# Kernel tuning notes

Hardware: AMD Instinct MI355X
Metric: run time of the kernel (lower is better)

The kernel has to match this reference:

```python
import jax, jax.numpy as jnp
import numpy as np

B, T, DSEQ = 4096, 128, 128
DMEAN, DPRIOR = 256, 256
H, DOUT = 256, 128
NEXP, SCALE = 4, 0.1
NUM_EDGES = max(1, int(B * B * 0.05))  # static top-k size


def setup_inputs() -> dict:
    key = jax.random.key(0)
    ks = jax.random.split(key, 20)
    def n(k, shape):
        return jax.random.normal(k, shape, dtype=jnp.float32) * 0.02
    z = lambda *s: jnp.zeros(s, jnp.float32)
    return {
        "input_seq": jax.random.normal(ks[0], (B, T, DSEQ), dtype=jnp.float32),
        "mean_embedding": jax.random.normal(ks[1], (B, DMEAN), dtype=jnp.float32),
        "prior_target": jax.random.normal(ks[2], (B, DPRIOR), dtype=jnp.float32),
        "gru_Wih0": n(ks[3], (3 * H, DSEQ)), "gru_Whh0": n(ks[4], (3 * H, H)),
        "gru_bih0": z(3 * H), "gru_bhh0": z(3 * H),
        "gru_Wih1": n(ks[5], (3 * H, H)), "gru_Whh1": n(ks[6], (3 * H, H)),
        "gru_bih1": z(3 * H), "gru_bhh1": z(3 * H),
        "fc_mean_W": n(ks[7], (H, DMEAN)), "fc_mean_b": z(H),
        "gru_fc_W": n(ks[8], (DOUT, 2 * H)), "gru_fc_b": z(DOUT),
        "gcn1_W": n(ks[9], (H, DPRIOR)), "gcn1_b": z(H),
        "gcn2_W": n(ks[10], (H, H)), "gcn2_b": z(H),
        "prior_fc_W": n(ks[11], (DOUT, H)), "prior_fc_b": z(DOUT),
        "expert_W": n(ks[12], (NEXP, DOUT, DOUT)),
        "attn1_W": n(ks[13], (DOUT, 2 * DOUT)), "attn1_b": z(DOUT),
        "attn2_W": n(ks[14], (NEXP, DOUT)), "attn2_b": z(NEXP),
    }


def _gru_layer(x, Wih, Whh, bih, bhh):
    # x: [B,T,D]; PyTorch GRU cell equations
    h_dim = Whh.shape[1]
    def step(h, xt):
        gi = xt @ Wih.T + bih            # [B,3H]
        gh = h @ Whh.T + bhh
        i_r, i_z, i_n = jnp.split(gi, 3, axis=-1)
        h_r, h_z, h_n = jnp.split(gh, 3, axis=-1)
        r = jax.nn.sigmoid(i_r + h_r)
        zg = jax.nn.sigmoid(i_z + h_z)
        ng = jnp.tanh(i_n + r * h_n)
        h_new = (1.0 - zg) * ng + zg * h
        return h_new, h_new
    h0 = jnp.zeros((x.shape[0], h_dim), x.dtype)
    _, ys = jax.lax.scan(step, h0, jnp.swapaxes(x, 0, 1))
    return jnp.swapaxes(ys, 0, 1)


def _gcn(x, W, b, src, dst, n_nodes):
    # PyG GCNConv: add self-loops, sym-normalized mean aggregation
    loop = jnp.arange(n_nodes)
    s = jnp.concatenate([src, loop])
    d = jnp.concatenate([dst, loop])
    deg = jax.ops.segment_sum(jnp.ones(s.shape, x.dtype), d, num_segments=n_nodes)
    dinv = jnp.where(deg > 0, jax.lax.rsqrt(deg), 0.0)
    norm = dinv[s] * dinv[d]                  # [E]
    xw = x @ W.T                              # [N,H]
    out = jax.ops.segment_sum(xw[s] * norm[:, None], d, num_segments=n_nodes)
    return out + b


def reference(input_seq, mean_embedding, prior_target,
              gru_Wih0, gru_Whh0, gru_bih0, gru_bhh0,
              gru_Wih1, gru_Whh1, gru_bih1, gru_bhh1,
              fc_mean_W, fc_mean_b, gru_fc_W, gru_fc_b,
              gcn1_W, gcn1_b, gcn2_W, gcn2_b,
              prior_fc_W, prior_fc_b, expert_W,
              attn1_W, attn1_b, attn2_W, attn2_b):
    # --- GRU branch ---
    h1 = _gru_layer(input_seq, gru_Wih0, gru_Whh0, gru_bih0, gru_bhh0)
    h2 = _gru_layer(h1, gru_Wih1, gru_Whh1, gru_bih1, gru_bhh1)
    last_hidden = h2[:, -1, :]
    mean_feat = jax.nn.relu(mean_embedding @ fc_mean_W.T + fc_mean_b)
    gru_feat = jnp.concatenate([last_hidden, mean_feat], axis=1)
    gru_out_proj = gru_feat @ gru_fc_W.T + gru_fc_b          # [B,DOUT]
    # --- dynamic graph build via similarity top-k ---
    sim = prior_target @ prior_target.T                      # [B,B]
    diag = jnp.arange(B)
    sim = sim.at[diag, diag].set(0.0)
    _, topk_idx = jax.lax.top_k(sim.reshape(-1), NUM_EDGES)
    row = topk_idx // B
    col = topk_idx % B
    src = jnp.concatenate([row, col])   # symmetrized edge list
    dst = jnp.concatenate([col, row])
    # --- GCN branch ---
    ph = jax.nn.relu(_gcn(prior_target, gcn1_W, gcn1_b, src, dst, B))
    ph = jax.nn.relu(_gcn(ph, gcn2_W, gcn2_b, src, dst, B))
    prior_out = ph @ prior_fc_W.T + prior_fc_b               # [B,DOUT]
    # --- attention expert gate fusion ---
    base = 0.5 * gru_out_proj + 0.5 * prior_out
    diff = gru_out_proj - prior_out
    expert_res = jnp.einsum('eod,bd->beo', expert_W, diff)   # [B,NEXP,DOUT]
    fused = jnp.concatenate([gru_out_proj, prior_out], axis=-1)
    hatt = jnp.tanh(fused @ attn1_W.T + attn1_b)
    w = jax.nn.softmax(hatt @ attn2_W.T + attn2_b, axis=-1)  # [B,NEXP]
    delta = jnp.einsum('be,beo->bo', w, expert_res)
    pred = base + SCALE * delta
    return pred, gru_out_proj, prior_out
```

## Files before the change

### kernel.cpp

```cpp
#include <hip/hip_runtime.h>
#include <hip/hip_bf16.h>

#define BB    4096
#define TT    128
#define DSEQ_ 128
#define HH    256
#define DOUT_ 128
#define NEXP_ 4
static const long NUM_EDGES_ = 838860;

typedef _Float16 f16;
typedef _Float16 f16x8 __attribute__((ext_vector_type(8)));
typedef float    f32x4 __attribute__((ext_vector_type(4)));

#define GLL(gp, lp) __builtin_amdgcn_global_load_lds( \
    (const __attribute__((address_space(1))) void*)(gp), \
    (__attribute__((address_space(3))) void*)(lp), 16, 0, 0)

__global__ void pack_weights_kernel(const float* __restrict__ Wih,
                                    const float* __restrict__ Whh,
                                    f16* __restrict__ Wp, int Din)
{
    const int K = Din + HH;
    const int total = 1024 * K;
    for (int idx = blockIdx.x * 256 + threadIdx.x; idx < total; idx += gridDim.x * 256) {
        int n = idx / K, k = idx % K;
        int u = n >> 2, g = n & 3;
        float v = 0.f;
        if (k < Din) {
            if (g == 0)      v = Wih[(long)u * Din + k];
            else if (g == 1) v = Wih[(long)(256 + u) * Din + k];
            else if (g == 2) v = Wih[(long)(512 + u) * Din + k];
        } else {
            int kh = k - Din;
            if (g == 0)      v = Whh[(long)u * HH + kh];
            else if (g == 1) v = Whh[(long)(256 + u) * HH + kh];
            else if (g == 3) v = Whh[(long)(512 + u) * HH + kh];
        }
        Wp[idx] = (f16)v;
    }
}

__global__ void pack_bias_kernel(const float* __restrict__ bih,
                                 const float* __restrict__ bhh,
                                 float* __restrict__ bias)
{
    int n = blockIdx.x * 256 + threadIdx.x;
    if (n >= 1024) return;
    int u = n >> 2, g = n & 3;
    float v;
    if (g == 0)      v = bih[u] + bhh[u];
    else if (g == 1) v = bih[256 + u] + bhh[256 + u];
    else if (g == 2) v = bih[512 + u];
    else             v = bhh[512 + u];
    bias[n] = v;
}

__device__ __forceinline__ void mm_async(
    f32x4 (&acc)[4][4], f16* __restrict__ As, f16* __restrict__ Bs,
    const f16* __restrict__ Ag, long lda, const f16* __restrict__ Bg, long ldb,
    int kChunks, int wave, int lane)
{
    const int r0 = wave * 32 + (lane >> 2);
    const int ce = (lane & 3) * 8;
    const int wm = wave >> 1, wn = wave & 1;
    const int quad = lane >> 4, l15 = lane & 15;
    const f16* ag0 = Ag + (long)r0 * lda + ce;
    const f16* ag1 = ag0 + 16 * lda;
    const f16* bg0 = Bg + (long)r0 * ldb + ce;
    const f16* bg1 = bg0 + 16 * ldb;
    f16* asw = As + wave * 1024;
    f16* bsw = Bs + wave * 1024;
    for (int kc = 0; kc < kChunks; kc++) {
        __syncthreads();
        GLL(ag0, asw); GLL(ag1, asw + 512);
        GLL(bg0, bsw); GLL(bg1, bsw + 512);
        ag0 += 32; ag1 += 32; bg0 += 32; bg1 += 32;
        __syncthreads();
        f16x8 af[4], bf[4];
#pragma unroll
        for (int i = 0; i < 4; i++) {
            af[i] = *(const f16x8*)&As[(wm * 64 + i * 16 + l15) * 32 + quad * 8];
            bf[i] = *(const f16x8*)&Bs[(wn * 64 + i * 16 + l15) * 32 + quad * 8];
        }
#pragma unroll
        for (int mi = 0; mi < 4; mi++)
#pragma unroll
            for (int ni = 0; ni < 4; ni++)
                acc[mi][ni] = __builtin_amdgcn_mfma_f32_16x16x32_f16(af[mi], bf[ni], acc[mi][ni], 0, 0, 0);
    }
}

__global__ __launch_bounds__(256) void gru_superstep(
    const f16* __restrict__ Wp0, const float* __restrict__ bias0,
    const float* __restrict__ xseq,
    const f16* __restrict__ h1_in, f16* __restrict__ h1_out, int t0,
    const f16* __restrict__ Wp1, const float* __restrict__ bias1,
    const f16* __restrict__ h1_x,
    const f16* __restrict__ h2_in, f16* __restrict__ h2_out, int t1)
{
    const int layer = blockIdx.z;
    if (layer == 0 && t0 >= TT) return;
    if (layer == 1 && t1 < 0) return;

    __shared__ f16 As[4096];
    __shared__ f16 Bs[4096];
    const int tid = threadIdx.x;
    const int wave = tid >> 6, lane = tid & 63;
    const int wm = wave >> 1, wn = wave & 1;
    const int quad = lane >> 4, l15 = lane & 15;
    const long m0 = (long)blockIdx.x * 128;
    const int  n0 = blockIdx.y * 128;

    f32x4 acc[4][4];
#pragma unroll
    for (int i = 0; i < 4; i++)
#pragma unroll
        for (int j = 0; j < 4; j++) acc[i][j] = (f32x4){0.f, 0.f, 0.f, 0.f};

    const f16* hprev; f16* hout; const float* bias;
    if (layer == 0) {
        hprev = h1_in; hout = h1_out; bias = bias0;
        const int arow = tid >> 1, ac0 = (tid & 1) * 16;
        const float* ap = xseq + (m0 + arow) * ((long)TT * DSEQ_) + (long)t0 * DSEQ_ + ac0;
        const int r0 = wave * 32 + (lane >> 2);
        const int ce = (lane & 3) * 8;
        const f16* bg0 = Wp0 + (long)(n0 + r0) * 384 + ce;
        const f16* bg1 = bg0 + 16 * 384;
        f16* bsw = Bs + wave * 1024;
        for (int kc = 0; kc < 4; kc++) {
            float4 v0 = *(const float4*)(ap + 0);
            float4 v1 = *(const float4*)(ap + 4);
            float4 v2 = *(const float4*)(ap + 8);
            float4 v3 = *(const float4*)(ap + 12);
            ap += 32;
            __syncthreads();
            f16x8 w0, w1;
            w0[0] = (f16)v0.x; w0[1] = (f16)v0.y; w0[2] = (f16)v0.z; w0[3] = (f16)v0.w;
            w0[4] = (f16)v1.x; w0[5] = (f16)v1.y; w0[6] = (f16)v1.z; w0[7] = (f16)v1.w;
            w1[0] = (f16)v2.x; w1[1] = (f16)v2.y; w1[2] = (f16)v2.z; w1[3] = (f16)v2.w;
            w1[4] = (f16)v3.x; w1[5] = (f16)v3.y; w1[6] = (f16)v3.z; w1[7] = (f16)v3.w;
            *(f16x8*)&As[arow * 32 + ac0]     = w0;
            *(f16x8*)&As[arow * 32 + ac0 + 8] = w1;
            GLL(bg0, bsw); GLL(bg1, bsw + 512);
            bg0 += 32; bg1 += 32;
            __syncthreads();
            f16x8 af[4], bf[4];
#pragma unroll
            for (int i = 0; i < 4; i++) {
                af[i] = *(const f16x8*)&As[(wm * 64 + i * 16 + l15) * 32 + quad * 8];
                bf[i] = *(const f16x8*)&Bs[(wn * 64 + i * 16 + l15) * 32 + quad * 8];
            }
#pragma unroll
            for (int mi = 0; mi < 4; mi++)
#pragma unroll
                for (int ni = 0; ni < 4; ni++)
                    acc[mi][ni] = __builtin_amdgcn_mfma_f32_16x16x32_f16(af[mi], bf[ni], acc[mi][ni], 0, 0, 0);
        }
        mm_async(acc, As, Bs, h1_in + m0 * HH, HH, Wp0 + (long)n0 * 384 + 128, 384, 8, wave, lane);
    } else {
        hprev = h2_in; hout = h2_out; bias = bias1;
        mm_async(acc, As, Bs, h1_x + m0 * HH, HH, Wp1 + (long)n0 * 512, 512, 8, wave, lane);
        mm_async(acc, As, Bs, h2_in + m0 * HH, HH, Wp1 + (long)n0 * 512 + 256, 512, 8, wave, lane);
    }

    const long mbase = m0 + wm * 64;
    const int  nbase = n0 + wn * 64;
#pragma unroll
    for (int mi = 0; mi < 4; mi++) {
#pragma unroll
        for (int ni = 0; ni < 4; ni++) {
            const int ncol = nbase + ni * 16 + l15;
            const float bn = bias[ncol];
#pragma unroll
            for (int reg = 0; reg < 4; reg++) {
                float v = acc[mi][ni][reg] + bn;
                const int gb = lane & ~3;
                float g0 = __shfl(v, gb + 0, 64);
                float g1 = __shfl(v, gb + 1, 64);
                float g2 = __shfl(v, gb + 2, 64);
                float g3 = __shfl(v, gb + 3, 64);
                if ((lane & 3) == 0) {
                    const long mrow = mbase + mi * 16 + quad * 4 + reg;
                    const int u = ncol >> 2;
                    float hp = (float)hprev[mrow * HH + u];
                    float r = 1.f / (1.f + __expf(-g0));
                    float z = 1.f / (1.f + __expf(-g1));
                    float ng = 1.f - 2.f / (__expf(2.f * (g2 + r * g3)) + 1.f);
                    float hn = (1.f - z) * ng + z * hp;
                    hout[mrow * HH + u] = (f16)hn;
                }
            }
        }
    }
}

__global__ void sim_pack_kernel(const float* __restrict__ prior,
                                f16* __restrict__ pA, f16* __restrict__ pB)
{
    int i = blockIdx.x * 256 + threadIdx.x;
    if (i >= BB * 256) return;
    int b = i >> 8, k = i & 255;
    float v = prior[i];
    f16 hi = (f16)v;
    f16 lo = (f16)(v - (float)hi);
    long r = (long)b * 768;
    pA[r + k] = hi; pA[r + 256 + k] = hi; pA[r + 512 + k] = lo;
    pB[r + k] = hi; pB[r + 256 + k] = lo; pB[r + 512 + k] = hi;
}

__global__ __launch_bounds__(256) void sim_mm_kernel(
    const f16* __restrict__ pA, const f16* __restrict__ pB, float* __restrict__ sim)
{
    __shared__ f16 As[4096];
    __shared__ f16 Bs[4096];
    const int tid = threadIdx.x;
    const int wave = tid >> 6, lane = tid & 63;
    const int wm = wave >> 1, wn = wave & 1;
    const int quad = lane >> 4, l15 = lane & 15;
    const long m0 = (long)blockIdx.x * 128;
    const int  n0 = blockIdx.y * 128;
    f32x4 acc[4][4];
#pragma unroll
    for (int i = 0; i < 4; i++)
#pragma unroll
        for (int j = 0; j < 4; j++) acc[i][j] = (f32x4){0.f, 0.f, 0.f, 0.f};
    mm_async(acc, As, Bs, pA + m0 * 768, 768, pB + (long)n0 * 768, 768, 24, wave, lane);
    const long mbase = m0 + wm * 64;
    const int  nbase = n0 + wn * 64;
#pragma unroll
    for (int mi = 0; mi < 4; mi++)
#pragma unroll
        for (int ni = 0; ni < 4; ni++)
#pragma unroll
            for (int reg = 0; reg < 4; reg++) {
                long row = mbase + mi * 16 + quad * 4 + reg;
                int col = nbase + ni * 16 + l15;
                float v = acc[mi][ni][reg];
                if (row == (long)col) v = 0.f;
                sim[row * BB + col] = v;
            }
}

__device__ inline unsigned keyOf(float f)
{
    unsigned u = __float_as_uint(f);
    return (u & 0x80000000u) ? ~u : (u | 0x80000000u);
}

__global__ void hist_kernel(const float* __restrict__ sim, unsigned* __restrict__ hist,
                            const unsigned* __restrict__ state, int pass)
{
    __shared__ unsigned h[4096];
    for (int i = threadIdx.x; i < 4096; i += 256) h[i] = 0;
    __syncthreads();
    unsigned pfx1 = 0, pfx2 = 0;
    if (pass == 1) pfx1 = state[0];
    if (pass == 2) pfx2 = state[2];
    const long ntot = (long)BB * BB;
    for (long i = (long)blockIdx.x * 256 + threadIdx.x; i < ntot; i += (long)gridDim.x * 256) {
        unsigned key = keyOf(sim[i]);
        if (pass == 0) atomicAdd(&h[key >> 20], 1u);
        else if (pass == 1) { if ((key >> 20) == pfx1) atomicAdd(&h[(key >> 8) & 0xFFFu], 1u); }
        else               { if ((key >> 8) == pfx2)  atomicAdd(&h[key & 0xFFu], 1u); }
    }
    __syncthreads();
    const int nb = (pass == 2) ? 256 : 4096;
    for (int i = threadIdx.x; i < nb; i += 256)
        if (h[i]) atomicAdd(&hist[i], h[i]);
}

__global__ void scan_hist_kernel(const unsigned* __restrict__ hist,
                                 unsigned* __restrict__ state, int pass)
{
    __shared__ unsigned hl[4096];
    const int nb = (pass == 2) ? 256 : 4096;
    for (int i = threadIdx.x; i < nb; i += 256) hl[i] = hist[i];
    __syncthreads();
    if (threadIdx.x != 0 || blockIdx.x != 0) return;
    long k = (pass == 0) ? NUM_EDGES_ : (long)state[2 * pass - 1];
    long cum = 0; int b = nb - 1;
    for (; b >= 0; b--) { cum += hl[b]; if (cum >= k) break; }
    long kk = k - (cum - hl[b]);
    if (pass == 0) { state[0] = (unsigned)b; state[1] = (unsigned)kk; }
    else if (pass == 1) { state[2] = (state[0] << 12) | (unsigned)b; state[3] = (unsigned)kk; }
    else {
        unsigned key = (state[2] << 8) | (unsigned)b;
        state[4] = key;
        unsigned u = (key & 0x80000000u) ? (key ^ 0x80000000u) : ~key;
        state[5] = u;
    }
}

__global__ void degree_kernel(const float* __restrict__ sim, const unsigned* __restrict__ state,
                              float* __restrict__ dinv)
{
    const float thr = __uint_as_float(state[5]);
    const int d = blockIdx.x;
    const float* row = sim + (long)d * BB;
    int cnt = 0;
    for (int s = threadIdx.x; s < BB; s += 256) cnt += (row[s] >= thr) ? 1 : 0;
    for (int o = 32; o; o >>= 1) cnt += __shfl_down(cnt, o, 64);
    __shared__ int sh[4];
    if ((threadIdx.x & 63) == 0) sh[threadIdx.x >> 6] = cnt;
    __syncthreads();
    if (threadIdx.x == 0) {
        int tot = sh[0] + sh[1] + sh[2] + sh[3];
        dinv[d] = rsqrtf((float)(2 * tot + 1));
    }
}

__global__ void txp_kernel(const float* __restrict__ xws, f16* __restrict__ bT)
{
    int i = blockIdx.x * 256 + threadIdx.x;
    if (i >= BB * 256) return;
    int n = i >> 12, m = i & 4095;
    bT[(long)n * BB + m] = (f16)xws[(long)m * 256 + n];
}

__global__ __launch_bounds__(256) void gcn_mm_kernel(
    const float* __restrict__ sim, const f16* __restrict__ bT,
    const unsigned* __restrict__ state, float* __restrict__ ps)
{
    const float thr = __uint_as_float(state[5]);
    __shared__ f16 As[4096];
    __shared__ f16 Bs[4096];
    const int tid = threadIdx.x;
    const int wave = tid >> 6, lane = tid & 63;
    const int wm = wave >> 1, wn = wave & 1;
    const int quad = lane >> 4, l15 = lane & 15;
    const long m0 = (long)blockIdx.x * 128;
    const int  n0 = blockIdx.y * 128;
    const long kbase = (long)blockIdx.z * 1024;
    f32x4 acc[4][4];
#pragma unroll
    for (int i = 0; i < 4; i++)
#pragma unroll
        for (int j = 0; j < 4; j++) acc[i][j] = (f32x4){0.f, 0.f, 0.f, 0.f};

    const int arow = tid >> 1, ac0 = (tid & 1) * 16;
    const float* ap = sim + (m0 + arow) * (long)BB + kbase + ac0;
    const int r0 = wave * 32 + (lane >> 2);
    const int ce = (lane & 3) * 8;
    const f16* bg0 = bT + (long)(n0 + r0) * BB + kbase + ce;
    const f16* bg1 = bg0 + 16 * BB;
    f16* bsw = Bs + wave * 1024;
    const f16 one = (f16)1.f, zero = (f16)0.f;
    for (int kc = 0; kc < 32; kc++) {
        float4 v0 = *(const float4*)(ap + 0);
        float4 v1 = *(const float4*)(ap + 4);
        float4 v2 = *(const float4*)(ap + 8);
        float4 v3 = *(const float4*)(ap + 12);
        ap += 32;
        __syncthreads();
        f16x8 w0, w1;
        w0[0] = v0.x >= thr ? one : zero; w0[1] = v0.y >= thr ? one : zero;
        w0[2] = v0.z >= thr ? one : zero; w0[3] = v0.w >= thr ? one : zero;
        w0[4] = v1.x >= thr ? one : zero; w0[5] = v1.y >= thr ? one : zero;
        w0[6] = v1.z >= thr ? one : zero; w0[7] = v1.w >= thr ? one : zero;
        w1[0] = v2.x >= thr ? one : zero; w1[1] = v2.y >= thr ? one : zero;
        w1[2] = v2.z >= thr ? one : zero; w1[3] = v2.w >= thr ? one : zero;
        w1[4] = v3.x >= thr ? one : zero; w1[5] = v3.y >= thr ? one : zero;
        w1[6] = v3.z >= thr ? one : zero; w1[7] = v3.w >= thr ? one : zero;
        *(f16x8*)&As[arow * 32 + ac0]     = w0;
        *(f16x8*)&As[arow * 32 + ac0 + 8] = w1;
        GLL(bg0, bsw); GLL(bg1, bsw + 512);
        bg0 += 32; bg1 += 32;
        __syncthreads();
        f16x8 af[4], bf[4];
#pragma unroll
        for (int i = 0; i < 4; i++) {
            af[i] = *(const f16x8*)&As[(wm * 64 + i * 16 + l15) * 32 + quad * 8];
            bf[i] = *(const f16x8*)&Bs[(wn * 64 + i * 16 + l15) * 32 + quad * 8];
        }
#pragma unroll
        for (int mi = 0; mi < 4; mi++)
#pragma unroll
            for (int ni = 0; ni < 4; ni++)
                acc[mi][ni] = __builtin_amdgcn_mfma_f32_16x16x32_f16(af[mi], bf[ni], acc[mi][ni], 0, 0, 0);
    }
    const long mbase = m0 + wm * 64;
    const int  nbase = n0 + wn * 64;
    float* pbase = ps + (long)blockIdx.z * BB * 256;
#pragma unroll
    for (int mi = 0; mi < 4; mi++)
#pragma unroll
        for (int ni = 0; ni < 4; ni++)
#pragma unroll
            for (int reg = 0; reg < 4; reg++) {
                long row = mbase + mi * 16 + quad * 4 + reg;
                int col = nbase + ni * 16 + l15;
                pbase[row * 256 + col] = acc[mi][ni][reg];
            }
}

__global__ void gcn_combine_kernel(const float* __restrict__ ps, const float* __restrict__ xws,
                                   const float* __restrict__ dinv, const float* __restrict__ b,
                                   float* __restrict__ out)
{
    const long S = (long)BB * 256;
    long i = (long)blockIdx.x * 256 + threadIdx.x;
    if (i >= S) return;
    float s = ps[i] + ps[i + S] + ps[i + 2 * S] + ps[i + 3 * S];
    long m = i >> 8; int n = (int)(i & 255);
    out[i] = fmaxf(dinv[m] * (2.f * s + xws[i]) + b[n], 0.f);
}

__global__ __launch_bounds__(256) void gemm_bt_kernel(
    const float* __restrict__ A, const float* __restrict__ Bm, float* __restrict__ C,
    int M, int N, int K, const float* __restrict__ bias,
    const float* __restrict__ rscale, int act)
{
    __shared__ float As[16][65];
    __shared__ float Bs[16][65];
    const int tid = threadIdx.x;
    const long m0 = (long)blockIdx.x * 64;
    const int  n0 = blockIdx.y * 64;
    const int ty = tid >> 4, tx = tid & 15;
    const int mA = tid >> 2, kq = (tid & 3) * 4;
    float c[4][4] = {};
    for (int k0 = 0; k0 < K; k0 += 16) {
        __syncthreads();
        float4 va = *(const float4*)&A[(m0 + mA) * K + k0 + kq];
        As[kq + 0][mA] = va.x; As[kq + 1][mA] = va.y; As[kq + 2][mA] = va.z; As[kq + 3][mA] = va.w;
        float4 vb = *(const float4*)&Bm[(long)(n0 + mA) * K + k0 + kq];
        Bs[kq + 0][mA] = vb.x; Bs[kq + 1][mA] = vb.y; Bs[kq + 2][mA] = vb.z; Bs[kq + 3][mA] = vb.w;
        __syncthreads();
#pragma unroll
        for (int k = 0; k < 16; k++) {
            float a4[4], b4[4];
#pragma unroll
            for (int j = 0; j < 4; j++) { a4[j] = As[k][ty * 4 + j]; b4[j] = Bs[k][tx * 4 + j]; }
#pragma unroll
            for (int i = 0; i < 4; i++)
#pragma unroll
                for (int j = 0; j < 4; j++) c[i][j] = fmaf(a4[i], b4[j], c[i][j]);
        }
    }
#pragma unroll
    for (int i = 0; i < 4; i++) {
        const long m = m0 + ty * 4 + i;
        const float rs = rscale ? rscale[m] : 1.f;
#pragma unroll
        for (int j = 0; j < 4; j++) {
            const int n = n0 + tx * 4 + j;
            float v = c[i][j] * rs;
            if (bias) v += bias[n];
            if (act == 1) v = fmaxf(v, 0.f);
            else if (act == 2) v = tanhf(v);
            C[m * N + n] = v;
        }
    }
}

__global__ void build_gru_feat_kernel(const f16* __restrict__ h2, const float* __restrict__ mf,
                                      float* __restrict__ gf)
{
    long i = (long)blockIdx.x * 256 + threadIdx.x;
    if (i >= (long)BB * 512) return;
    long b = i >> 9; int c = (int)(i & 511);
    gf[i] = (c < 256) ? (float)h2[b * HH + c] : mf[b * HH + (c - 256)];
}

__global__ void build_fused_diff_kernel(const float* __restrict__ g, const float* __restrict__ p,
                                        float* __restrict__ fused, float* __restrict__ diff)
{
    long i = (long)blockIdx.x * 256 + threadIdx.x;
    if (i >= (long)BB * 256) return;
    long b = i >> 8; int c = (int)(i & 255);
    if (c < 128) {
        float gv = g[b * 128 + c], pv = p[b * 128 + c];
        fused[i] = gv;
        diff[b * 128 + c] = gv - pv;
    } else {
        fused[i] = p[b * 128 + (c - 128)];
    }
}

__global__ __launch_bounds__(128) void final_kernel(
    const float* __restrict__ hatt, const float* __restrict__ attn2W, const float* __restrict__ attn2b,
    const float* __restrict__ er, const float* __restrict__ g, const float* __restrict__ p,
    float* __restrict__ pred)
{
    const int b = blockIdx.x;
    __shared__ float w4[4];
    __shared__ float hrow[128];
    const int tid = threadIdx.x;
    hrow[tid] = hatt[(long)b * 128 + tid];
    __syncthreads();
    if (tid < 4) {
        float s = attn2b[tid];
        for (int d = 0; d < 128; d++) s += hrow[d] * attn2W[tid * 128 + d];
        w4[tid] = s;
    }
    __syncthreads();
    if (tid == 0) {
        float mx = fmaxf(fmaxf(w4[0], w4[1]), fmaxf(w4[2], w4[3]));
        float e0 = __expf(w4[0] - mx), e1 = __expf(w4[1] - mx);
        float e2 = __expf(w4[2] - mx), e3 = __expf(w4[3] - mx);
        float inv = 1.f / (e0 + e1 + e2 + e3);
        w4[0] = e0 * inv; w4[1] = e1 * inv; w4[2] = e2 * inv; w4[3] = e3 * inv;
    }
    __syncthreads();
    const long off = (long)b * 128 + tid;
    const long E = (long)BB * DOUT_;
    float base = 0.5f * g[off] + 0.5f * p[off];
    float delta = w4[0] * er[off] + w4[1] * er[off + E] + w4[2] * er[off + 2 * E] + w4[3] * er[off + 3 * E];
    pred[off] = base + 0.1f * delta;
}

extern "C" void kernel_launch(void* const* d_in, const int* in_sizes, int n_in,
                              void* d_out, int out_size, void* d_ws, size_t ws_size,
                              hipStream_t stream)
{
    const float* input_seq  = (const float*)d_in[0];
    const float* mean_emb   = (const float*)d_in[1];
    const float* prior      = (const float*)d_in[2];
    const float* Wih0       = (const float*)d_in[3];
    const float* Whh0       = (const float*)d_in[4];
    const float* bih0       = (const float*)d_in[5];
    const float* bhh0       = (const float*)d_in[6];
    const float* Wih1       = (const float*)d_in[7];
    const float* Whh1       = (const float*)d_in[8];
    const float* bih1       = (const float*)d_in[9];
    const float* bhh1       = (const float*)d_in[10];
    const float* fc_mean_W  = (const float*)d_in[11];
    const float* fc_mean_b  = (const float*)d_in[12];
    const float* gru_fc_W   = (const float*)d_in[13];
    const float* gru_fc_b   = (const float*)d_in[14];
    const float* gcn1_W     = (const float*)d_in[15];
    const float* gcn1_b     = (const float*)d_in[16];
    const float* gcn2_W     = (const float*)d_in[17];
    const float* gcn2_b     = (const float*)d_in[18];
    const float* prior_fc_W = (const float*)d_in[19];
    const float* prior_fc_b = (const float*)d_in[20];
    const float* expert_W   = (const float*)d_in[21];
    const float* attn1_W    = (const float*)d_in[22];
    const float* attn1_b    = (const float*)d_in[23];
    const float* attn2_W    = (const float*)d_in[24];
    const float* attn2_b    = (const float*)d_in[25];

    float* out_pred = (float*)d_out;
    float* out_g    = out_pred + (long)BB * DOUT_;
    float* out_p    = out_g + (long)BB * DOUT_;

    const size_t MB = 1u << 20;
    char* base = (char*)d_ws;
    size_t off = 0;
    auto alloc = [&](size_t bytes) -> char* {
        char* p = base + off;
        off = (off + bytes + 255) & ~(size_t)255;
        return p;
    };
    f16*   wp0    = (f16*)alloc((size_t)1024 * 384 * 2);
    f16*   wp1    = (f16*)alloc((size_t)1024 * 512 * 2);
    float* bias0  = (float*)alloc(1024 * 4);
    float* bias1  = (float*)alloc(1024 * 4);
    f16*   h1b[2]; h1b[0] = (f16*)alloc((size_t)BB * HH * 2); h1b[1] = (f16*)alloc((size_t)BB * HH * 2);
    f16*   h2b[2]; h2b[0] = (f16*)alloc((size_t)BB * HH * 2); h2b[1] = (f16*)alloc((size_t)BB * HH * 2);
    float* sim    = (float*)alloc((size_t)BB * BB * 4);
    unsigned* hist  = (unsigned*)alloc(4096 * 4);
    unsigned* state = (unsigned*)alloc(256);
    float* dinv   = (float*)alloc(BB * 4);
    float* xws1   = (float*)alloc((size_t)BB * HH * 4);
    float* ph1    = (float*)alloc((size_t)BB * HH * 4);
    float* xws2   = (float*)alloc((size_t)BB * HH * 4);
    float* ph2    = (float*)alloc((size_t)BB * HH * 4);
    f16*   xwsT16 = (f16*)alloc((size_t)256 * BB * 2);
    char*  region = alloc(20 * MB);
    if (off > ws_size) return;

    float* mf     = (float*)(region);
    float* gf     = (float*)(region + 5 * MB);
    f16*   packA  = (f16*)(region);
    f16*   packB  = (f16*)(region + 7 * MB);
    float* ps     = (float*)(region);
    float* diffb  = (float*)(region);
    float* fusedb = (float*)(region + 3 * MB);
    float* hatt   = (float*)(region + 8 * MB);
    float* er     = (float*)(region + 11 * MB);

    pack_weights_kernel<<<1536, 256, 0, stream>>>(Wih0, Whh0, wp0, DSEQ_);
    pack_weights_kernel<<<2048, 256, 0, stream>>>(Wih1, Whh1, wp1, HH);
    pack_bias_kernel<<<4, 256, 0, stream>>>(bih0, bhh0, bias0);
    pack_bias_kernel<<<4, 256, 0, stream>>>(bih1, bhh1, bias1);
    hipMemsetAsync(h1b[0], 0, (size_t)BB * HH * 2, stream);
    hipMemsetAsync(h1b[1], 0, (size_t)BB * HH * 2, stream);
    hipMemsetAsync(h2b[0], 0, (size_t)BB * HH * 2, stream);
    hipMemsetAsync(h2b[1], 0, (size_t)BB * HH * 2, stream);

    for (int tau = 0; tau <= TT; tau++) {
        gru_superstep<<<dim3(32, 8, 2), 256, 0, stream>>>(
            wp0, bias0, input_seq, h1b[tau & 1], h1b[(tau + 1) & 1], tau,
            wp1, bias1, h1b[tau & 1], h2b[tau & 1], h2b[(tau + 1) & 1], tau - 1);
    }
    const f16* h2fin = h2b[(TT + 1) & 1];

    gemm_bt_kernel<<<dim3(64, 4), 256, 0, stream>>>(mean_emb, fc_mean_W, mf, BB, HH, 256, fc_mean_b, nullptr, 1);
    build_gru_feat_kernel<<<(BB * 512) / 256, 256, 0, stream>>>(h2fin, mf, gf);
    gemm_bt_kernel<<<dim3(64, 2), 256, 0, stream>>>(gf, gru_fc_W, out_g, BB, DOUT_, 512, gru_fc_b, nullptr, 0);

    sim_pack_kernel<<<4096, 256, 0, stream>>>(prior, packA, packB);
    sim_mm_kernel<<<dim3(32, 32), 256, 0, stream>>>(packA, packB, sim);
    for (int pass = 0; pass < 3; pass++) {
        hipMemsetAsync(hist, 0, 4096 * 4, stream);
        hist_kernel<<<1024, 256, 0, stream>>>(sim, hist, state, pass);
        scan_hist_kernel<<<1, 256, 0, stream>>>(hist, state, pass);
    }
    degree_kernel<<<BB, 256, 0, stream>>>(sim, state, dinv);

    gemm_bt_kernel<<<dim3(64, 4), 256, 0, stream>>>(prior, gcn1_W, xws1, BB, HH, 256, nullptr, dinv, 0);
    txp_kernel<<<4096, 256, 0, stream>>>(xws1, xwsT16);
    gcn_mm_kernel<<<dim3(32, 2, 4), 256, 0, stream>>>(sim, xwsT16, state, ps);
    gcn_combine_kernel<<<4096, 256, 0, stream>>>(ps, xws1, dinv, gcn1_b, ph1);
    gemm_bt_kernel<<<dim3(64, 4), 256, 0, stream>>>(ph1, gcn2_W, xws2, BB, HH, 256, nullptr, dinv, 0);
    txp_kernel<<<4096, 256, 0, stream>>>(xws2, xwsT16);
    gcn_mm_kernel<<<dim3(32, 2, 4), 256, 0, stream>>>(sim, xwsT16, state, ps);
    gcn_combine_kernel<<<4096, 256, 0, stream>>>(ps, xws2, dinv, gcn2_b, ph2);
    gemm_bt_kernel<<<dim3(64, 2), 256, 0, stream>>>(ph2, prior_fc_W, out_p, BB, DOUT_, 256, prior_fc_b, nullptr, 0);

    build_fused_diff_kernel<<<(BB * 256) / 256, 256, 0, stream>>>(out_g, out_p, fusedb, diffb);
    for (int e = 0; e < NEXP_; e++)
        gemm_bt_kernel<<<dim3(64, 2), 256, 0, stream>>>(diffb, expert_W + (long)e * DOUT_ * DOUT_,
                                                        er + (long)e * BB * DOUT_, BB, DOUT_, DOUT_,
                                                        nullptr, nullptr, 0);
    gemm_bt_kernel<<<dim3(64, 2), 256, 0, stream>>>(fusedb, attn1_W, hatt, BB, DOUT_, 256, attn1_b, nullptr, 2);
    final_kernel<<<BB, 128, 0, stream>>>(hatt, attn2_W, attn2_b, er, out_g, out_p, out_pred);
}
```

Measured before the change: 5.198 ms.

## Replace per-timestep GRU launches with persistent cooperative kernel holding weights in LDS

Replaces the 129 per-timestep GRU kernel launches with a single cooperative persistent kernel of 256 blocks. Each block keeps its 128-row weight slice resident in LDS for all timesteps, double-buffers the activation tiles, and uses a grid-wide sync between steps. This removes launch overhead and the repeated reloading of weights from global memory, at the cost of grid.sync latency, one block per CU, and up to 144KB of LDS per block. The top-k histogram scan is also rewritten as a single-wave parallel prefix scan using ballots instead of a serial single-thread loop.

Result: slower. 12.92 ms (+148.6%).

```diff
diff --git a/kernel.cpp b/kernel.cpp
--- a/kernel.cpp
+++ b/kernel.cpp
@@ -1,5 +1,8 @@
 #include <hip/hip_runtime.h>
 #include <hip/hip_bf16.h>
+#include <hip/hip_cooperative_groups.h>
+
+namespace cg = cooperative_groups;
 
 #define BB    4096
 #define TT    128
@@ -56,6 +59,164 @@
     bias[n] = v;
 }
 
+__device__ __forceinline__ void stage_h(const f16* __restrict__ src, f16* __restrict__ buf,
+                                        int wave, int lane)
+{
+    const int r0 = wave * 32 + (lane >> 2);
+    const int ce = (lane & 3) * 8;
+    const f16* g0 = src + (long)r0 * HH + ce;
+    GLL(g0, buf + wave * 1024);
+    GLL(g0 + 16 * HH, buf + wave * 1024 + 512);
+}
+
+__device__ __forceinline__ void cvt_store(const float4* xr, f16* __restrict__ dst)
+{
+    f16x8 w0, w1;
+    w0[0] = (f16)xr[0].x; w0[1] = (f16)xr[0].y; w0[2] = (f16)xr[0].z; w0[3] = (f16)xr[0].w;
+    w0[4] = (f16)xr[1].x; w0[5] = (f16)xr[1].y; w0[6] = (f16)xr[1].z; w0[7] = (f16)xr[1].w;
+    w1[0] = (f16)xr[2].x; w1[1] = (f16)xr[2].y; w1[2] = (f16)xr[2].z; w1[3] = (f16)xr[2].w;
+    w1[4] = (f16)xr[3].x; w1[5] = (f16)xr[3].y; w1[6] = (f16)xr[3].z; w1[7] = (f16)xr[3].w;
+    *(f16x8*)dst       = w0;
+    *(f16x8*)(dst + 8) = w1;
+}
+
+__global__ __launch_bounds__(256, 1) void gru_persistent(
+    const f16* __restrict__ Wp0, const float* __restrict__ bias0,
+    const float* __restrict__ xseq,
+    const f16* __restrict__ Wp1, const float* __restrict__ bias1,
+    f16* __restrict__ h1p0, f16* __restrict__ h1p1,
+    f16* __restrict__ h2p0, f16* __restrict__ h2p1)
+{
+    cg::grid_group grid = cg::this_grid();
+    __shared__ f16 Bw[16 * 128 * 32];
+    __shared__ f16 As[2][4096];
+
+    const int tid  = threadIdx.x;
+    const int wave = tid >> 6, lane = tid & 63;
+    const int wm = wave >> 1, wn = wave & 1;
+    const int quad = lane >> 4, l15 = lane & 15;
+    const int b = blockIdx.x;
+    const int layer = b >> 7;
+    const int lb = b & 127;
+    const int nb = lb >> 4;
+    const int mg = lb & 15;
+    const int n0 = nb * 128;
+    const int K0  = layer ? 512 : 384;
+    const int nch = K0 >> 5;
+    const int nxch = layer ? 0 : 4;
+    const f16* Wp = layer ? Wp1 : Wp0;
+    const float* bias = layer ? bias1 : bias0;
+
+    const int upr = K0 >> 3;
+    for (int i = tid; i < 128 * upr; i += 256) {
+        int r = i / upr, u = i % upr;
+        int kc = u >> 2, c8 = u & 3;
+        f16x8 v = *(const f16x8*)&Wp[(long)(n0 + r) * K0 + kc * 32 + c8 * 8];
+        *(f16x8*)&Bw[kc * 4096 + r * 32 + c8 * 8] = v;
+    }
+    __syncthreads();
+
+    const int arow = tid >> 1, ac0 = (tid & 1) * 16;
+
+    for (int tau = 0; tau <= TT; tau++) {
+        const bool active = layer ? (tau >= 1) : (tau < TT);
+        if (active) {
+            const int t = layer ? (tau - 1) : tau;
+            const f16* h1r = (tau & 1) ? h1p1 : h1p0;
+            f16*       h1w = (tau & 1) ? h1p0 : h1p1;
+            const f16* h2r = (tau & 1) ? h2p1 : h2p0;
+            f16*       h2w = (tau & 1) ? h2p0 : h2p1;
+            const f16* hprev = layer ? h2r : h1r;
+            f16*       hout  = layer ? h2w : h1w;
+            const float* xrow0 = xseq + (long)t * DSEQ_ + ac0;
+
+            for (int mt = 0; mt < 2; mt++) {
+                const long m0 = ((long)(mg * 2 + mt)) * 128;
+                f32x4 acc[4][4];
+#pragma unroll
+                for (int i = 0; i < 4; i++)
+#pragma unroll
+                    for (int j = 0; j < 4; j++) acc[i][j] = (f32x4){0.f, 0.f, 0.f, 0.f};
+
+                float4 xr[4];
+                if (layer == 0) {
+                    const float* ap = xrow0 + (m0 + arow) * (long)(TT * DSEQ_);
+                    xr[0] = *(const float4*)(ap + 0);
+                    xr[1] = *(const float4*)(ap + 4);
+                    xr[2] = *(const float4*)(ap + 8);
+                    xr[3] = *(const float4*)(ap + 12);
+                } else {
+                    stage_h(h1r + m0 * HH, As[0], wave, lane);
+                }
+
+                for (int kc = 0; kc < nch; kc++) {
+                    const int cur = kc & 1, nxt = cur ^ 1;
+                    if (kc < nxch) cvt_store(xr, &As[cur][arow * 32 + ac0]);
+                    __syncthreads();
+                    const int kn = kc + 1;
+                    if (kn < nch) {
+                        if (kn < nxch) {
+                            const float* ap = xrow0 + (m0 + arow) * (long)(TT * DSEQ_) + kn * 32;
+                            xr[0] = *(const float4*)(ap + 0);
+                            xr[1] = *(const float4*)(ap + 4);
+                            xr[2] = *(const float4*)(ap + 8);
+                            xr[3] = *(const float4*)(ap + 12);
+                        } else {
+                            const f16* src; long coff;
+                            if (layer == 0)   { src = h1r; coff = (kn - 4) * 32; }
+                            else if (kn < 8)  { src = h1r; coff = kn * 32; }
+                            else              { src = h2r; coff = (kn - 8) * 32; }
+                            stage_h(src + m0 * HH + coff, As[nxt], wave, lane);
+                        }
+                    }
+                    f16x8 af[4], bf[4];
+#pragma unroll
+                    for (int i = 0; i < 4; i++) {
+                        af[i] = *(const f16x8*)&As[cur][(wm * 64 + i * 16 + l15) * 32 + quad * 8];
+                        bf[i] = *(const f16x8*)&Bw[kc * 4096 + (wn * 64 + i * 16 + l15) * 32 + quad * 8];
+                    }
+#pragma unroll
+                    for (int mi = 0; mi < 4; mi++)
+#pragma unroll
+                        for (int ni = 0; ni < 4; ni++)
+                            acc[mi][ni] = __builtin_amdgcn_mfma_f32_16x16x32_f16(af[mi], bf[ni], acc[mi][ni], 0, 0, 0);
+                }
+
+                const long mbase = m0 + wm * 64;
+                const int  nbase = n0 + wn * 64;
+#pragma unroll
+                for (int mi = 0; mi < 4; mi++)
+#pragma unroll
+                    for (int ni = 0; ni < 4; ni++) {
+                        const int ncol = nbase + ni * 16 + l15;
+                        const float bn = bias[ncol];
+#pragma unroll
+                        for (int reg = 0; reg < 4; reg++) {
+                            float v = acc[mi][ni][reg] + bn;
+                            const int gb = lane & ~3;
+                            float g0 = __shfl(v, gb + 0, 64);
+                            float g1 = __shfl(v, gb + 1, 64);
+                            float g2 = __shfl(v, gb + 2, 64);
+                            float g3 = __shfl(v, gb + 3, 64);
+                            if ((lane & 3) == 0) {
+                                const long mrow = mbase + mi * 16 + quad * 4 + reg;
+                                const int u = ncol >> 2;
+                                float hp = (float)hprev[mrow * HH + u];
+                                float r = 1.f / (1.f + __expf(-g0));
+                                float z = 1.f / (1.f + __expf(-g1));
+                                float ng = 1.f - 2.f / (__expf(2.f * (g2 + r * g3)) + 1.f);
+                                float hn = (1.f - z) * ng + z * hp;
+                                hout[mrow * HH + u] = (f16)hn;
+                            }
+                        }
+                    }
+            }
+        }
+        __threadfence();
+        grid.sync();
+    }
+}
+
 __device__ __forceinline__ void mm_async(
     f32x4 (&acc)[4][4], f16* __restrict__ As, f16* __restrict__ Bs,
     const f16* __restrict__ Ag, long lda, const f16* __restrict__ Bg, long ldb,
@@ -91,110 +252,6 @@
     }
 }
 
-__global__ __launch_bounds__(256) void gru_superstep(
-    const f16* __restrict__ Wp0, const float* __restrict__ bias0,
-    const float* __restrict__ xseq,
-    const f16* __restrict__ h1_in, f16* __restrict__ h1_out, int t0,
-    const f16* __restrict__ Wp1, const float* __restrict__ bias1,
-    const f16* __restrict__ h1_x,
-    const f16* __restrict__ h2_in, f16* __restrict__ h2_out, int t1)
-{
-    const int layer = blockIdx.z;
-    if (layer == 0 && t0 >= TT) return;
-    if (layer == 1 && t1 < 0) return;
-
-    __shared__ f16 As[4096];
-    __shared__ f16 Bs[4096];
-    const int tid = threadIdx.x;
-    const int wave = tid >> 6, lane = tid & 63;
-    const int wm = wave >> 1, wn = wave & 1;
-    const int quad = lane >> 4, l15 = lane & 15;
-    const long m0 = (long)blockIdx.x * 128;
-    const int  n0 = blockIdx.y * 128;
-
-    f32x4 acc[4][4];
-#pragma unroll
-    for (int i = 0; i < 4; i++)
-#pragma unroll
-        for (int j = 0; j < 4; j++) acc[i][j] = (f32x4){0.f, 0.f, 0.f, 0.f};
-
-    const f16* hprev; f16* hout; const float* bias;
-    if (layer == 0) {
-        hprev = h1_in; hout = h1_out; bias = bias0;
-        const int arow = tid >> 1, ac0 = (tid & 1) * 16;
-        const float* ap = xseq + (m0 + arow) * ((long)TT * DSEQ_) + (long)t0 * DSEQ_ + ac0;
-        const int r0 = wave * 32 + (lane >> 2);
-        const int ce = (lane & 3) * 8;
-        const f16* bg0 = Wp0 + (long)(n0 + r0) * 384 + ce;
-        const f16* bg1 = bg0 + 16 * 384;
-        f16* bsw = Bs + wave * 1024;
-        for (int kc = 0; kc < 4; kc++) {
-            float4 v0 = *(const float4*)(ap + 0);
-            float4 v1 = *(const float4*)(ap + 4);
-            float4 v2 = *(const float4*)(ap + 8);
-            float4 v3 = *(const float4*)(ap + 12);
-            ap += 32;
-            __syncthreads();
-            f16x8 w0, w1;
-            w0[0] = (f16)v0.x; w0[1] = (f16)v0.y; w0[2] = (f16)v0.z; w0[3] = (f16)v0.w;
-            w0[4] = (f16)v1.x; w0[5] = (f16)v1.y; w0[6] = (f16)v1.z; w0[7] = (f16)v1.w;
-            w1[0] = (f16)v2.x; w1[1] = (f16)v2.y; w1[2] = (f16)v2.z; w1[3] = (f16)v2.w;
-            w1[4] = (f16)v3.x; w1[5] = (f16)v3.y; w1[6] = (f16)v3.z; w1[7] = (f16)v3.w;
-            *(f16x8*)&As[arow * 32 + ac0]     = w0;
-            *(f16x8*)&As[arow * 32 + ac0 + 8] = w1;
-            GLL(bg0, bsw); GLL(bg1, bsw + 512);
-            bg0 += 32; bg1 += 32;
-            __syncthreads();
-            f16x8 af[4], bf[4];
-#pragma unroll
-            for (int i = 0; i < 4; i++) {
-                af[i] = *(const f16x8*)&As[(wm * 64 + i * 16 + l15) * 32 + quad * 8];
-                bf[i] = *(const f16x8*)&Bs[(wn * 64 + i * 16 + l15) * 32 + quad * 8];
-            }
-#pragma unroll
-            for (int mi = 0; mi < 4; mi++)
-#pragma unroll
-                for (int ni = 0; ni < 4; ni++)
-                    acc[mi][ni] = __builtin_amdgcn_mfma_f32_16x16x32_f16(af[mi], bf[ni], acc[mi][ni], 0, 0, 0);
-        }
-        mm_async(acc, As, Bs, h1_in + m0 * HH, HH, Wp0 + (long)n0 * 384 + 128, 384, 8, wave, lane);
-    } else {
-        hprev = h2_in; hout = h2_out; bias = bias1;
-        mm_async(acc, As, Bs, h1_x + m0 * HH, HH, Wp1 + (long)n0 * 512, 512, 8, wave, lane);
-        mm_async(acc, As, Bs, h2_in + m0 * HH, HH, Wp1 + (long)n0 * 512 + 256, 512, 8, wave, lane);
-    }
-
-    const long mbase = m0 + wm * 64;
-    const int  nbase = n0 + wn * 64;
-#pragma unroll
-    for (int mi = 0; mi < 4; mi++) {
-#pragma unroll
-        for (int ni = 0; ni < 4; ni++) {
-            const int ncol = nbase + ni * 16 + l15;
-            const float bn = bias[ncol];
-#pragma unroll
-            for (int reg = 0; reg < 4; reg++) {
-                float v = acc[mi][ni][reg] + bn;
-                const int gb = lane & ~3;
-                float g0 = __shfl(v, gb + 0, 64);
-                float g1 = __shfl(v, gb + 1, 64);
-                float g2 = __shfl(v, gb + 2, 64);
-                float g3 = __shfl(v, gb + 3, 64);
-                if ((lane & 3) == 0) {
-                    const long mrow = mbase + mi * 16 + quad * 4 + reg;
-                    const int u = ncol >> 2;
-                    float hp = (float)hprev[mrow * HH + u];
-                    float r = 1.f / (1.f + __expf(-g0));
-                    float z = 1.f / (1.f + __expf(-g1));
-                    float ng = 1.f - 2.f / (__expf(2.f * (g2 + r * g3)) + 1.f);
-                    float hn = (1.f - z) * ng + z * hp;
-                    hout[mrow * HH + u] = (f16)hn;
-                }
-            }
-        }
-    }
-}
-
 __global__ void sim_pack_kernel(const float* __restrict__ prior,
                                 f16* __restrict__ pA, f16* __restrict__ pB)
 {
@@ -273,22 +330,44 @@
 __global__ void scan_hist_kernel(const unsigned* __restrict__ hist,
                                  unsigned* __restrict__ state, int pass)
 {
-    __shared__ unsigned hl[4096];
+    const int lane = threadIdx.x;
     const int nb = (pass == 2) ? 256 : 4096;
-    for (int i = threadIdx.x; i < nb; i += 256) hl[i] = hist[i];
-    __syncthreads();
-    if (threadIdx.x != 0 || blockIdx.x != 0) return;
-    long k = (pass == 0) ? NUM_EDGES_ : (long)state[2 * pass - 1];
-    long cum = 0; int b = nb - 1;
-    for (; b >= 0; b--) { cum += hl[b]; if (cum >= k) break; }
-    long kk = k - (cum - hl[b]);
-    if (pass == 0) { state[0] = (unsigned)b; state[1] = (unsigned)kk; }
-    else if (pass == 1) { state[2] = (state[0] << 12) | (unsigned)b; state[3] = (unsigned)kk; }
-    else {
-        unsigned key = (state[2] << 8) | (unsigned)b;
-        state[4] = key;
-        unsigned u = (key & 0x80000000u) ? (key ^ 0x80000000u) : ~key;
-        state[5] = u;
+    const int seg = nb >> 6;
+    const unsigned k = (pass == 0) ? (unsigned)NUM_EDGES_ : state[2 * pass - 1];
+
+    unsigned local = 0;
+    for (int j = 0; j < seg; j++) local += hist[lane * seg + j];
+    unsigned T = local;
+#pragma unroll
+    for (int off = 1; off < 64; off <<= 1) {
+        unsigned tv = __shfl_down(T, off, 64);
+        if (lane + off < 64) T += tv;
+    }
+    unsigned long long m1 = __ballot(T >= k);
+    const int Ls = 63 - __builtin_clzll(m1);
+    unsigned Tnext = 0;
+    if (Ls < 63) Tnext = __shfl(T, Ls + 1, 64);
+
+    unsigned v = (lane < seg) ? hist[Ls * seg + lane] : 0u;
+    unsigned S = v;
+#pragma unroll
+    for (int off = 1; off < 64; off <<= 1) {
+        unsigned tv = __shfl_down(S, off, 64);
+        if (lane + off < 64) S += tv;
+    }
+    unsigned long long m2 = __ballot(Tnext + S >= k);
+    const int js = 63 - __builtin_clzll(m2);
+    if (lane == js) {
+        const int bsel = Ls * seg + js;
+        const unsigned kk = k - Tnext - (S - v);
+        if (pass == 0)      { state[0] = (unsigned)bsel; state[1] = kk; }
+        else if (pass == 1) { state[2] = (state[0] << 12) | (unsigned)bsel; state[3] = kk; }
+        else {
+            unsigned key = (state[2] << 8) | (unsigned)bsel;
+            state[4] = key;
+            unsigned u = (key & 0x80000000u) ? (key ^ 0x80000000u) : ~key;
+            state[5] = u;
+        }
     }
 }
 
@@ -589,10 +668,12 @@
     hipMemsetAsync(h2b[0], 0, (size_t)BB * HH * 2, stream);
     hipMemsetAsync(h2b[1], 0, (size_t)BB * HH * 2, stream);
 
-    for (int tau = 0; tau <= TT; tau++) {
-        gru_superstep<<<dim3(32, 8, 2), 256, 0, stream>>>(
-            wp0, bias0, input_seq, h1b[tau & 1], h1b[(tau + 1) & 1], tau,
-            wp1, bias1, h1b[tau & 1], h2b[tau & 1], h2b[(tau + 1) & 1], tau - 1);
+    {
+        const f16* a0 = wp0; const float* a1 = bias0; const float* a2 = input_seq;
+        const f16* a3 = wp1; const float* a4 = bias1;
+        f16* a5 = h1b[0]; f16* a6 = h1b[1]; f16* a7 = h2b[0]; f16* a8 = h2b[1];
+        void* args[] = {&a0, &a1, &a2, &a3, &a4, &a5, &a6, &a7, &a8};
+        hipLaunchCooperativeKernel((void*)gru_persistent, dim3(256), dim3(256), args, 0, stream);
     }
     const f16* h2fin = h2b[(TT + 1) & 1];
 
@@ -605,7 +686,7 @@
     for (int pass = 0; pass < 3; pass++) {
         hipMemsetAsync(hist, 0, 4096 * 4, stream);
         hist_kernel<<<1024, 256, 0, stream>>>(sim, hist, state, pass);
-        scan_hist_kernel<<<1, 256, 0, stream>>>(hist, state, pass);
+        scan_hist_kernel<<<1, 64, 0, stream>>>(hist, state, pass);
     }
     degree_kernel<<<BB, 256, 0, stream>>>(sim, state, dinv);
 
```
